# Kernel tuning notes

Hardware: AMD Instinct MI355X
Metric: run time of the kernel (lower is better)

## Reference

```python
import jax, jax.numpy as jnp
import numpy as np

B, C, K, D = 16, 128, 128, 256
EPS = 1e-5  # torch BatchNorm1d default eps


def _bn(x, gamma, beta):
    # torch BatchNorm1d training-mode on (N, ch, L): normalize each channel over (N, L)
    mean = x.mean(axis=(0, 2), keepdims=True)
    var = x.var(axis=(0, 2), keepdims=True)  # biased, matches torch normalization
    return (x - mean) / jnp.sqrt(var + EPS) * gamma[None, :, None] + beta[None, :, None]


def setup_inputs() -> dict:
    key = jax.random.key(0)
    ks = jax.random.split(key, 6)
    q = jax.random.normal(ks[0], (B, C, D), jnp.float32)
    kc = jax.random.normal(ks[1], (B, K, D), jnp.float32)
    W0 = jax.random.normal(ks[2], (D, D), jnp.float32) / np.sqrt(D)
    W1 = jax.random.normal(ks[3], (D, D), jnp.float32) / np.sqrt(D)
    cmask = jax.random.randint(ks[4], (B, C), 0, 2, jnp.int32)
    kmask = jax.random.randint(ks[5], (B, K), 0, 2, jnp.int32)
    klen = jnp.maximum(kmask.sum(axis=1), 1).astype(jnp.int32)
    return {
        "query_candidates_repr": q,
        "key_candidates": kc,
        "W0": W0,
        "W1": W1,
        "bn0_gamma": jnp.ones((C,), jnp.float32),
        "bn0_beta": jnp.zeros((C,), jnp.float32),
        "bn1_gamma": jnp.ones((K,), jnp.float32),
        "bn1_beta": jnp.zeros((K,), jnp.float32),
        "query_candidate_mask": cmask,
        "key_candidate_mask": kmask,
        "key_candidate_len": klen,
    }


def reference(query_candidates_repr, key_candidates, W0, W1,
              bn0_gamma, bn0_beta, bn1_gamma, bn1_beta,
              query_candidate_mask, key_candidate_mask, key_candidate_len):
    # gated_attention branch (att_type != 'softmax'), activate = tanh
    g0 = _bn(query_candidates_repr @ W0.T, bn0_gamma, bn0_beta)  # (B,C,D)
    g1 = _bn(key_candidates @ W1.T, bn1_gamma, bn1_beta)          # (B,K,D)
    # (B,C,K,D) gate product
    attention_weight = jax.nn.sigmoid(g1)[:, None, :, :] * jax.nn.sigmoid(g0)[:, :, None, :]
    attention_res = key_candidates[:, None, :, :] * attention_weight  # (B,C,K,D)
    mask = (query_candidate_mask[:, :, None] * key_candidate_mask[:, None, :]).astype(jnp.float32)
    attention_res_masked = attention_res * mask[..., None]
    attention_vector = attention_res_masked.sum(axis=2) / key_candidate_len[:, None, None].astype(jnp.float32)
    output_res = jnp.tanh(attention_vector)  # (B,C,D)
    return output_res, attention_res_masked, attention_weight.mean(axis=-1)
```

## Files before the change

kernel.cpp:

```cpp
#include <hip/hip_runtime.h>


#define NB 16
#define NC 128
#define NK 128
#define ND 256

__global__ __launch_bounds__(256) void k_gemm(const float* __restrict__ q,
                                              const float* __restrict__ kc,
                                              const float* __restrict__ W0,
                                              const float* __restrict__ W1,
                                              float* __restrict__ Y) {
    __shared__ float As[16][64];
    __shared__ float Bs[16][64];
    const int m0 = blockIdx.x * 64;
    const int d0 = blockIdx.y * 64;
    const int t  = threadIdx.x;
    const float* A = (m0 < 2048) ? (q + (size_t)m0 * ND) : (kc + (size_t)(m0 - 2048) * ND);
    const float* W = (m0 < 2048) ? W0 : W1;
    const int ml = t >> 2;
    const int jl = (t & 3) * 4;
    const int ty = t >> 4;
    const int tx = t & 15;

    float acc[4][4] = {};
    for (int j0 = 0; j0 < 256; j0 += 16) {
        float4 a = *(const float4*)(A + ml * ND + j0 + jl);
        float4 b = *(const float4*)(W + (d0 + ml) * ND + j0 + jl);
        As[jl + 0][ml] = a.x; As[jl + 1][ml] = a.y; As[jl + 2][ml] = a.z; As[jl + 3][ml] = a.w;
        Bs[jl + 0][ml] = b.x; Bs[jl + 1][ml] = b.y; Bs[jl + 2][ml] = b.z; Bs[jl + 3][ml] = b.w;
        __syncthreads();
#pragma unroll
        for (int jj = 0; jj < 16; ++jj) {
            float4 av = *(const float4*)&As[jj][ty * 4];
            float4 bv = *(const float4*)&Bs[jj][tx * 4];
            acc[0][0] += av.x * bv.x; acc[0][1] += av.x * bv.y; acc[0][2] += av.x * bv.z; acc[0][3] += av.x * bv.w;
            acc[1][0] += av.y * bv.x; acc[1][1] += av.y * bv.y; acc[1][2] += av.y * bv.z; acc[1][3] += av.y * bv.w;
            acc[2][0] += av.z * bv.x; acc[2][1] += av.z * bv.y; acc[2][2] += av.z * bv.z; acc[2][3] += av.z * bv.w;
            acc[3][0] += av.w * bv.x; acc[3][1] += av.w * bv.y; acc[3][2] += av.w * bv.z; acc[3][3] += av.w * bv.w;
        }
        __syncthreads();
    }
#pragma unroll
    for (int i = 0; i < 4; ++i) {
        float4 o = make_float4(acc[i][0], acc[i][1], acc[i][2], acc[i][3]);
        *(float4*)(Y + (size_t)(m0 + ty * 4 + i) * ND + d0 + tx * 4) = o;
    }
}

__global__ __launch_bounds__(256) void k_stats(const float* __restrict__ Y,
                                               const float* __restrict__ g0, const float* __restrict__ b0,
                                               const float* __restrict__ g1, const float* __restrict__ b1,
                                               float* __restrict__ sc, float* __restrict__ sh) {
    const int ch = blockIdx.x;
    const int t  = threadIdx.x;
    const int rbase = (ch < 128) ? ch : (2048 + (ch - 128));
    float s = 0.f, s2 = 0.f;
#pragma unroll
    for (int b = 0; b < NB; ++b) {
        float v = Y[(size_t)(rbase + b * 128) * ND + t];
        s += v; s2 += v * v;
    }
#pragma unroll
    for (int off = 32; off > 0; off >>= 1) {
        s  += __shfl_down(s,  off, 64);
        s2 += __shfl_down(s2, off, 64);
    }
    __shared__ float r1[4], r2[4];
    const int w = t >> 6;
    if ((t & 63) == 0) { r1[w] = s; r2[w] = s2; }
    __syncthreads();
    if (t == 0) {
        s  = r1[0] + r1[1] + r1[2] + r1[3];
        s2 = r2[0] + r2[1] + r2[2] + r2[3];
        float mean = s * (1.f / 4096.f);
        float var  = s2 * (1.f / 4096.f) - mean * mean;
        float rstd = rsqrtf(var + 1e-5f);
        float g  = (ch < 128) ? g0[ch] : g1[ch - 128];
        float be = (ch < 128) ? b0[ch] : b1[ch - 128];
        sc[ch] = g * rstd;
        sh[ch] = be - mean * g * rstd;
    }
}

__global__ __launch_bounds__(256) void k_apply(float* __restrict__ Y,
                                               const float* __restrict__ sc, const float* __restrict__ sh) {
    const int m = blockIdx.x;
    const int t = threadIdx.x;
    const size_t idx = (size_t)m * ND + t;
    float x = Y[idx];
    const int ch = (m < 2048) ? (m & 127) : (128 + (m & 127));
    float g = x * sc[ch] + sh[ch];
    Y[idx] = 1.f / (1.f + __expf(-g));
}

__global__ __launch_bounds__(256) void k_big(const float* __restrict__ Y,
                                             const float* __restrict__ kc,
                                             const int* __restrict__ cmask,
                                             const int* __restrict__ kmask,
                                             const int* __restrict__ klen,
                                             float* __restrict__ out0,
                                             float* __restrict__ out1,
                                             float* __restrict__ out2) {
    const int bc = blockIdx.x;
    const int b  = bc >> 7;
    const int t  = threadIdx.x;
    const int f  = t & 63;
    const int g  = t >> 6;

    const float* s0row = Y + (size_t)bc * ND;
    const float* s1b   = Y + (size_t)(2048 + b * 128) * ND;
    const float* kcb   = kc + (size_t)b * 128 * ND;
    const int*   kmb   = kmask + b * 128;

    float4 s0v = *(const float4*)(s0row + f * 4);
    const bool cm = cmask[bc] != 0;
    float4 v0 = cm ? s0v : make_float4(0.f, 0.f, 0.f, 0.f);

    float tx_ = 0.f, ty_ = 0.f, tz_ = 0.f, tw_ = 0.f;
    const size_t o1base = (size_t)bc * 128 * ND;

    for (int k0 = 0; k0 < 32; ++k0) {
        const int k = k0 * 4 + g;
        float4 s1v = *(const float4*)(s1b + (size_t)k * ND + f * 4);
        float4 kcv = *(const float4*)(kcb + (size_t)k * ND + f * 4);
        const float km = (float)kmb[k];

        float4 uv = make_float4(km * kcv.x * s1v.x, km * kcv.y * s1v.y,
                                km * kcv.z * s1v.z, km * kcv.w * s1v.w);

        *(float4*)(out1 + o1base + (size_t)k * ND + f * 4) =
            make_float4(v0.x * uv.x, v0.y * uv.y, v0.z * uv.z, v0.w * uv.w);

        tx_ += uv.x; ty_ += uv.y; tz_ += uv.z; tw_ += uv.w;

        float dot = s0v.x * s1v.x + s0v.y * s1v.y + s0v.z * s1v.z + s0v.w * s1v.w;
#pragma unroll
        for (int off = 32; off > 0; off >>= 1) dot += __shfl_down(dot, off, 64);
        if (f == 0) out2[(size_t)bc * 128 + k] = dot * (1.f / 256.f);
    }

    __shared__ float tl[4][256];
    *(float4*)&tl[g][f * 4] = make_float4(tx_, ty_, tz_, tw_);
    __syncthreads();
    if (g == 0) {
        float4 t0 = *(const float4*)&tl[0][f * 4];
        float4 t1 = *(const float4*)&tl[1][f * 4];
        float4 t2 = *(const float4*)&tl[2][f * 4];
        float4 t3 = *(const float4*)&tl[3][f * 4];
        const float inv = 1.f / (float)klen[b];
        float ax = tanhf(v0.x * (t0.x + t1.x + t2.x + t3.x) * inv);
        float ay = tanhf(v0.y * (t0.y + t1.y + t2.y + t3.y) * inv);
        float az = tanhf(v0.z * (t0.z + t1.z + t2.z + t3.z) * inv);
        float aw = tanhf(v0.w * (t0.w + t1.w + t2.w + t3.w) * inv);
        *(float4*)(out0 + (size_t)bc * ND + f * 4) = make_float4(ax, ay, az, aw);
    }
}

extern "C" void kernel_launch(void* const* d_in, const int* in_sizes, int n_in,
                              void* d_out, int out_size, void* d_ws, size_t ws_size,
                              hipStream_t stream) {
    const float* q     = (const float*)d_in[0];
    const float* kc    = (const float*)d_in[1];
    const float* W0    = (const float*)d_in[2];
    const float* W1    = (const float*)d_in[3];
    const float* g0    = (const float*)d_in[4];
    const float* b0    = (const float*)d_in[5];
    const float* g1    = (const float*)d_in[6];
    const float* b1    = (const float*)d_in[7];
    const int*   cmask = (const int*)d_in[8];
    const int*   kmask = (const int*)d_in[9];
    const int*   klen  = (const int*)d_in[10];

    float* ws = (float*)d_ws;
    float* Y  = ws;
    float* sc = ws + 1048576;
    float* sh = ws + 1048832;

    float* o    = (float*)d_out;
    float* out0 = o;
    float* out1 = o + 524288;
    float* out2 = o + 67633152;

    k_gemm<<<dim3(64, 4), 256, 0, stream>>>(q, kc, W0, W1, Y);
    k_stats<<<256, 256, 0, stream>>>(Y, g0, b0, g1, b1, sc, sh);
    k_apply<<<4096, 256, 0, stream>>>(Y, sc, sh);
    k_big<<<2048, 256, 0, stream>>>(Y, kc, cmask, kmask, klen, out0, out1, out2);
}
```

Measured before the change: 321.0 us.

## Precompute masked key-gate product and split big kernel into per-output kernels

```diff
diff --git a/kernel.cpp b/kernel.cpp
--- a/kernel.cpp
+++ b/kernel.cpp
@@ -84,77 +84,97 @@
 }
 
 __global__ __launch_bounds__(256) void k_apply(float* __restrict__ Y,
-                                               const float* __restrict__ sc, const float* __restrict__ sh) {
+                                               const float* __restrict__ kc,
+                                               const int* __restrict__ kmask,
+                                               const float* __restrict__ sc, const float* __restrict__ sh,
+                                               float* __restrict__ u) {
     const int m = blockIdx.x;
     const int t = threadIdx.x;
     const size_t idx = (size_t)m * ND + t;
     float x = Y[idx];
     const int ch = (m < 2048) ? (m & 127) : (128 + (m & 127));
     float g = x * sc[ch] + sh[ch];
-    Y[idx] = 1.f / (1.f + __expf(-g));
-}
-
-__global__ __launch_bounds__(256) void k_big(const float* __restrict__ Y,
-                                             const float* __restrict__ kc,
-                                             const int* __restrict__ cmask,
-                                             const int* __restrict__ kmask,
-                                             const int* __restrict__ klen,
-                                             float* __restrict__ out0,
-                                             float* __restrict__ out1,
-                                             float* __restrict__ out2) {
+    float v = 1.f / (1.f + __expf(-g));
+    Y[idx] = v;
+    if (m >= 2048) {
+        const int mm = m - 2048;
+        float uu = kmask[mm] ? (kc[(size_t)mm * ND + t] * v) : 0.f;
+        u[(size_t)mm * ND + t] = uu;
+    }
+}
+
+__global__ __launch_bounds__(256) void k_tvec(const float* __restrict__ u,
+                                              float* __restrict__ tvec) {
+    const int b = blockIdx.x;
+    const int t = threadIdx.x;
+    const float* ub = u + (size_t)b * 128 * ND + t;
+    float s = 0.f;
+#pragma unroll 8
+    for (int k = 0; k < 128; ++k) s += ub[(size_t)k * ND];
+    tvec[b * ND + t] = s;
+}
+
+__global__ __launch_bounds__(256) void k_out2(const float* __restrict__ Y,
+                                              float* __restrict__ out2) {
     const int bc = blockIdx.x;
     const int b  = bc >> 7;
     const int t  = threadIdx.x;
     const int f  = t & 63;
     const int g  = t >> 6;
-
-    const float* s0row = Y + (size_t)bc * ND;
-    const float* s1b   = Y + (size_t)(2048 + b * 128) * ND;
-    const float* kcb   = kc + (size_t)b * 128 * ND;
-    const int*   kmb   = kmask + b * 128;
-
-    float4 s0v = *(const float4*)(s0row + f * 4);
-    const bool cm = cmask[bc] != 0;
-    float4 v0 = cm ? s0v : make_float4(0.f, 0.f, 0.f, 0.f);
-
-    float tx_ = 0.f, ty_ = 0.f, tz_ = 0.f, tw_ = 0.f;
-    const size_t o1base = (size_t)bc * 128 * ND;
-
+    const float* s1b = Y + (size_t)(2048 + b * 128) * ND;
+    float4 s0v = *(const float4*)(Y + (size_t)bc * ND + f * 4);
     for (int k0 = 0; k0 < 32; ++k0) {
         const int k = k0 * 4 + g;
         float4 s1v = *(const float4*)(s1b + (size_t)k * ND + f * 4);
-        float4 kcv = *(const float4*)(kcb + (size_t)k * ND + f * 4);
-        const float km = (float)kmb[k];
-
-        float4 uv = make_float4(km * kcv.x * s1v.x, km * kcv.y * s1v.y,
-                                km * kcv.z * s1v.z, km * kcv.w * s1v.w);
-
+        float dot = s0v.x * s1v.x + s0v.y * s1v.y + s0v.z * s1v.z + s0v.w * s1v.w;
+#pragma unroll
+        for (int off = 32; off > 0; off >>= 1) dot += __shfl_down(dot, off, 64);
+        if (f == 0) out2[(size_t)bc * 128 + k] = dot * (1.f / 256.f);
+    }
+}
+
+__global__ __launch_bounds__(256) void k_out1(const float* __restrict__ Y,
+                                              const float* __restrict__ u,
+                                              const int* __restrict__ cmask,
+                                              float* __restrict__ out1) {
+    const int bc = blockIdx.x;
+    const int b  = bc >> 7;
+    const int t  = threadIdx.x;
+    const int f  = t & 63;
+    const int g  = t >> 6;
+    float4 s0v = *(const float4*)(Y + (size_t)bc * ND + f * 4);
+    const bool cm = cmask[bc] != 0;
+    float4 v0 = cm ? s0v : make_float4(0.f, 0.f, 0.f, 0.f);
+    const float* ub = u + (size_t)b * 128 * ND;
+    const size_t o1base = (size_t)bc * 128 * ND;
+#pragma unroll 4
+    for (int k0 = 0; k0 < 32; ++k0) {
+        const int k = k0 * 4 + g;
+        float4 uv = *(const float4*)(ub + (size_t)k * ND + f * 4);
         *(float4*)(out1 + o1base + (size_t)k * ND + f * 4) =
             make_float4(v0.x * uv.x, v0.y * uv.y, v0.z * uv.z, v0.w * uv.w);
-
-        tx_ += uv.x; ty_ += uv.y; tz_ += uv.z; tw_ += uv.w;
-
-        float dot = s0v.x * s1v.x + s0v.y * s1v.y + s0v.z * s1v.z + s0v.w * s1v.w;
-#pragma unroll
-        for (int off = 32; off > 0; off >>= 1) dot += __shfl_down(dot, off, 64);
-        if (f == 0) out2[(size_t)bc * 128 + k] = dot * (1.f / 256.f);
-    }
-
-    __shared__ float tl[4][256];
-    *(float4*)&tl[g][f * 4] = make_float4(tx_, ty_, tz_, tw_);
-    __syncthreads();
-    if (g == 0) {
-        float4 t0 = *(const float4*)&tl[0][f * 4];
-        float4 t1 = *(const float4*)&tl[1][f * 4];
-        float4 t2 = *(const float4*)&tl[2][f * 4];
-        float4 t3 = *(const float4*)&tl[3][f * 4];
-        const float inv = 1.f / (float)klen[b];
-        float ax = tanhf(v0.x * (t0.x + t1.x + t2.x + t3.x) * inv);
-        float ay = tanhf(v0.y * (t0.y + t1.y + t2.y + t3.y) * inv);
-        float az = tanhf(v0.z * (t0.z + t1.z + t2.z + t3.z) * inv);
-        float aw = tanhf(v0.w * (t0.w + t1.w + t2.w + t3.w) * inv);
-        *(float4*)(out0 + (size_t)bc * ND + f * 4) = make_float4(ax, ay, az, aw);
-    }
+    }
+}
+
+__global__ __launch_bounds__(256) void k_out0(const float* __restrict__ Y,
+                                              const float* __restrict__ tvec,
+                                              const int* __restrict__ cmask,
+                                              const int* __restrict__ klen,
+                                              float* __restrict__ out0) {
+    const int idx = blockIdx.x * 256 + threadIdx.x;
+    const int bc  = idx >> 6;
+    const int f   = idx & 63;
+    const int b   = bc >> 7;
+    float4 s0v = *(const float4*)(Y + (size_t)bc * ND + f * 4);
+    float4 tv  = *(const float4*)(tvec + b * ND + f * 4);
+    const float sel = (cmask[bc] != 0) ? 1.f : 0.f;
+    const float inv = sel / (float)klen[b];
+    float4 o;
+    o.x = tanhf(s0v.x * tv.x * inv);
+    o.y = tanhf(s0v.y * tv.y * inv);
+    o.z = tanhf(s0v.z * tv.z * inv);
+    o.w = tanhf(s0v.w * tv.w * inv);
+    *(float4*)(out0 + (size_t)bc * ND + f * 4) = o;
 }
 
 extern "C" void kernel_launch(void* const* d_in, const int* in_sizes, int n_in,
@@ -172,10 +192,12 @@
     const int*   kmask = (const int*)d_in[9];
     const int*   klen  = (const int*)d_in[10];
 
-    float* ws = (float*)d_ws;
-    float* Y  = ws;
-    float* sc = ws + 1048576;
-    float* sh = ws + 1048832;
+    float* ws   = (float*)d_ws;
+    float* Y    = ws;
+    float* u    = ws + 1048576;
+    float* tvec = ws + 1572864;
+    float* sc   = ws + 1576960;
+    float* sh   = ws + 1577216;
 
     float* o    = (float*)d_out;
     float* out0 = o;
@@ -184,6 +206,9 @@
 
     k_gemm<<<dim3(64, 4), 256, 0, stream>>>(q, kc, W0, W1, Y);
     k_stats<<<256, 256, 0, stream>>>(Y, g0, b0, g1, b1, sc, sh);
-    k_apply<<<4096, 256, 0, stream>>>(Y, sc, sh);
-    k_big<<<2048, 256, 0, stream>>>(Y, kc, cmask, kmask, klen, out0, out1, out2);
-}
+    k_apply<<<4096, 256, 0, stream>>>(Y, kc, kmask, sc, sh, u);
+    k_tvec<<<16, 256, 0, stream>>>(u, tvec);
+    k_out2<<<2048, 256, 0, stream>>>(Y, out2);
+    k_out1<<<2048, 256, 0, stream>>>(Y, u, cmask, out1);
+    k_out0<<<512, 256, 0, stream>>>(Y, tvec, cmask, klen, out0);
+}
```

Measured after the change: 383.6 us. 19.5% more time.

## Precompute masked key gate product and compute mean-weight output via batched GEMM

Applied to the files above, without the earlier changes.

```diff
diff --git a/kernel.cpp b/kernel.cpp
--- a/kernel.cpp
+++ b/kernel.cpp
@@ -84,60 +84,94 @@
 }
 
 __global__ __launch_bounds__(256) void k_apply(float* __restrict__ Y,
-                                               const float* __restrict__ sc, const float* __restrict__ sh) {
+                                               const float* __restrict__ kc,
+                                               const int* __restrict__ kmask,
+                                               const float* __restrict__ sc, const float* __restrict__ sh,
+                                               float* __restrict__ u) {
     const int m = blockIdx.x;
     const int t = threadIdx.x;
     const size_t idx = (size_t)m * ND + t;
     float x = Y[idx];
     const int ch = (m < 2048) ? (m & 127) : (128 + (m & 127));
     float g = x * sc[ch] + sh[ch];
-    Y[idx] = 1.f / (1.f + __expf(-g));
-}
-
-__global__ __launch_bounds__(256) void k_big(const float* __restrict__ Y,
-                                             const float* __restrict__ kc,
-                                             const int* __restrict__ cmask,
-                                             const int* __restrict__ kmask,
-                                             const int* __restrict__ klen,
-                                             float* __restrict__ out0,
-                                             float* __restrict__ out1,
-                                             float* __restrict__ out2) {
+    float v = 1.f / (1.f + __expf(-g));
+    Y[idx] = v;
+    if (m >= 2048) {
+        const int mm = m - 2048;
+        float uu = kmask[mm] ? (kc[(size_t)mm * ND + t] * v) : 0.f;
+        u[(size_t)mm * ND + t] = uu;
+    }
+}
+
+__global__ __launch_bounds__(256) void k_out2gemm(const float* __restrict__ Y,
+                                                  float* __restrict__ out2) {
+    __shared__ float As[16][64];
+    __shared__ float Bs[16][64];
+    const int b  = blockIdx.x;
+    const int c0 = blockIdx.y * 64;
+    const int k0 = blockIdx.z * 64;
+    const int t  = threadIdx.x;
+    const float* A = Y + (size_t)(b * 128 + c0) * ND;
+    const float* W = Y + (size_t)(2048 + b * 128 + k0) * ND;
+    const int ml = t >> 2;
+    const int jl = (t & 3) * 4;
+    const int ty = t >> 4;
+    const int tx = t & 15;
+
+    float acc[4][4] = {};
+    for (int j0 = 0; j0 < 256; j0 += 16) {
+        float4 a = *(const float4*)(A + ml * ND + j0 + jl);
+        float4 w = *(const float4*)(W + ml * ND + j0 + jl);
+        As[jl + 0][ml] = a.x; As[jl + 1][ml] = a.y; As[jl + 2][ml] = a.z; As[jl + 3][ml] = a.w;
+        Bs[jl + 0][ml] = w.x; Bs[jl + 1][ml] = w.y; Bs[jl + 2][ml] = w.z; Bs[jl + 3][ml] = w.w;
+        __syncthreads();
+#pragma unroll
+        for (int jj = 0; jj < 16; ++jj) {
+            float4 av = *(const float4*)&As[jj][ty * 4];
+            float4 bv = *(const float4*)&Bs[jj][tx * 4];
+            acc[0][0] += av.x * bv.x; acc[0][1] += av.x * bv.y; acc[0][2] += av.x * bv.z; acc[0][3] += av.x * bv.w;
+            acc[1][0] += av.y * bv.x; acc[1][1] += av.y * bv.y; acc[1][2] += av.y * bv.z; acc[1][3] += av.y * bv.w;
+            acc[2][0] += av.z * bv.x; acc[2][1] += av.z * bv.y; acc[2][2] += av.z * bv.z; acc[2][3] += av.z * bv.w;
+            acc[3][0] += av.w * bv.x; acc[3][1] += av.w * bv.y; acc[3][2] += av.w * bv.z; acc[3][3] += av.w * bv.w;
+        }
+        __syncthreads();
+    }
+    float* ob = out2 + (size_t)b * 128 * 128;
+#pragma unroll
+    for (int i = 0; i < 4; ++i) {
+        float4 o = make_float4(acc[i][0] * (1.f / 256.f), acc[i][1] * (1.f / 256.f),
+                               acc[i][2] * (1.f / 256.f), acc[i][3] * (1.f / 256.f));
+        *(float4*)(ob + (size_t)(c0 + ty * 4 + i) * 128 + k0 + tx * 4) = o;
+    }
+}
+
+__global__ __launch_bounds__(256) void k_big2(const float* __restrict__ Y,
+                                              const float* __restrict__ u,
+                                              const int* __restrict__ cmask,
+                                              const int* __restrict__ klen,
+                                              float* __restrict__ out0,
+                                              float* __restrict__ out1) {
     const int bc = blockIdx.x;
     const int b  = bc >> 7;
     const int t  = threadIdx.x;
     const int f  = t & 63;
     const int g  = t >> 6;
 
-    const float* s0row = Y + (size_t)bc * ND;
-    const float* s1b   = Y + (size_t)(2048 + b * 128) * ND;
-    const float* kcb   = kc + (size_t)b * 128 * ND;
-    const int*   kmb   = kmask + b * 128;
-
-    float4 s0v = *(const float4*)(s0row + f * 4);
+    float4 s0v = *(const float4*)(Y + (size_t)bc * ND + f * 4);
     const bool cm = cmask[bc] != 0;
     float4 v0 = cm ? s0v : make_float4(0.f, 0.f, 0.f, 0.f);
 
+    const float* ub = u + (size_t)b * 128 * ND;
+    const size_t o1base = (size_t)bc * 128 * ND;
+
     float tx_ = 0.f, ty_ = 0.f, tz_ = 0.f, tw_ = 0.f;
-    const size_t o1base = (size_t)bc * 128 * ND;
-
+#pragma unroll 8
     for (int k0 = 0; k0 < 32; ++k0) {
         const int k = k0 * 4 + g;
-        float4 s1v = *(const float4*)(s1b + (size_t)k * ND + f * 4);
-        float4 kcv = *(const float4*)(kcb + (size_t)k * ND + f * 4);
-        const float km = (float)kmb[k];
-
-        float4 uv = make_float4(km * kcv.x * s1v.x, km * kcv.y * s1v.y,
-                                km * kcv.z * s1v.z, km * kcv.w * s1v.w);
-
+        float4 uv = *(const float4*)(ub + (size_t)k * ND + f * 4);
         *(float4*)(out1 + o1base + (size_t)k * ND + f * 4) =
             make_float4(v0.x * uv.x, v0.y * uv.y, v0.z * uv.z, v0.w * uv.w);
-
         tx_ += uv.x; ty_ += uv.y; tz_ += uv.z; tw_ += uv.w;
-
-        float dot = s0v.x * s1v.x + s0v.y * s1v.y + s0v.z * s1v.z + s0v.w * s1v.w;
-#pragma unroll
-        for (int off = 32; off > 0; off >>= 1) dot += __shfl_down(dot, off, 64);
-        if (f == 0) out2[(size_t)bc * 128 + k] = dot * (1.f / 256.f);
     }
 
     __shared__ float tl[4][256];
@@ -174,8 +208,9 @@
 
     float* ws = (float*)d_ws;
     float* Y  = ws;
-    float* sc = ws + 1048576;
-    float* sh = ws + 1048832;
+    float* u  = ws + 1048576;
+    float* sc = ws + 1572864;
+    float* sh = ws + 1573120;
 
     float* o    = (float*)d_out;
     float* out0 = o;
@@ -184,6 +219,7 @@
 
     k_gemm<<<dim3(64, 4), 256, 0, stream>>>(q, kc, W0, W1, Y);
     k_stats<<<256, 256, 0, stream>>>(Y, g0, b0, g1, b1, sc, sh);
-    k_apply<<<4096, 256, 0, stream>>>(Y, sc, sh);
-    k_big<<<2048, 256, 0, stream>>>(Y, kc, cmask, kmask, klen, out0, out1, out2);
-}
+    k_apply<<<4096, 256, 0, stream>>>(Y, kc, kmask, sc, sh, u);
+    k_out2gemm<<<dim3(16, 2, 2), 256, 0, stream>>>(Y, out2);
+    k_big2<<<2048, 256, 0, stream>>>(Y, u, cmask, klen, out0, out1);
+}
```

Result: slower. 333.9 us (+4.0%).
